# Kernel optimization log

Hardware: AMD Instinct MI355X
Metric: run time of the kernel (lower is better)

## Reference

```python
import jax, jax.numpy as jnp
import numpy as np
import math

D_MODEL = 1024
N_HEADS = 16
D_HEAD = 64
D_MLP = 4096
N_LAYERS = 12
INIT_STD = 0.02
EPS = 1e-5
BATCH = 2
SEQ = 2048


def setup_inputs() -> dict:
    key = jax.random.key(0)
    ks = jax.random.split(key, 8)
    attn_std = INIT_STD
    proj_std = INIT_STD / math.sqrt(2 * N_LAYERS)
    return {
        "resid_pre": jax.random.normal(ks[0], (BATCH, SEQ, D_MODEL), jnp.float32),
        "ln1_w": jnp.ones((D_MODEL,), jnp.float32),
        "ln1_b": jnp.zeros((D_MODEL,), jnp.float32),
        "W_Q": attn_std * jax.random.normal(ks[1], (N_HEADS, D_MODEL, D_HEAD), jnp.float32),
        "b_Q": jnp.zeros((N_HEADS, D_HEAD), jnp.float32),
        "W_K": attn_std * jax.random.normal(ks[2], (N_HEADS, D_MODEL, D_HEAD), jnp.float32),
        "b_K": jnp.zeros((N_HEADS, D_HEAD), jnp.float32),
        "W_V": attn_std * jax.random.normal(ks[3], (N_HEADS, D_MODEL, D_HEAD), jnp.float32),
        "b_V": jnp.zeros((N_HEADS, D_HEAD), jnp.float32),
        "W_O": proj_std * jax.random.normal(ks[4], (N_HEADS, D_HEAD, D_MODEL), jnp.float32),
        "b_O": jnp.zeros((D_MODEL,), jnp.float32),
        "ln2_w": jnp.ones((D_MODEL,), jnp.float32),
        "ln2_b": jnp.zeros((D_MODEL,), jnp.float32),
        "W_in": INIT_STD * jax.random.normal(ks[5], (D_MODEL, D_MLP), jnp.float32),
        "b_in": jnp.zeros((D_MLP,), jnp.float32),
        "W_out": proj_std * jax.random.normal(ks[6], (D_MLP, D_MODEL), jnp.float32),
        "b_out": jnp.zeros((D_MODEL,), jnp.float32),
    }


def _layernorm(x, w, b):
    mean = x.mean(-1, keepdims=True)
    var = x.var(-1, keepdims=True)  # unbiased=False
    return (x - mean) / jnp.sqrt(var + EPS) * w + b


def _attention(x, W_Q, b_Q, W_K, b_K, W_V, b_V, W_O, b_O):
    # x: [b, s, d]; W_*: [h, d, k]
    q = jnp.einsum('bsd,hdk->bshk', x, W_Q) + b_Q
    k = jnp.einsum('bsd,hdk->bshk', x, W_K) + b_K
    v = jnp.einsum('bsd,hdk->bshk', x, W_V) + b_V
    scores = jnp.einsum('bqhk,bshk->bhqs', q, k) / math.sqrt(D_HEAD)
    seq = x.shape[1]
    causal = jnp.tril(jnp.ones((seq, seq), bool))
    scores = jnp.where(causal, scores, -jnp.inf)
    pattern = jax.nn.softmax(scores, axis=-1)
    z = jnp.einsum('bhqs,bshk->bqhk', pattern, v)
    return jnp.einsum('bqhk,hkd->bqd', z, W_O) + b_O


def reference(resid_pre, ln1_w, ln1_b, W_Q, b_Q, W_K, b_K, W_V, b_V, W_O, b_O,
              ln2_w, ln2_b, W_in, b_in, W_out, b_out):
    attn_out = _attention(_layernorm(resid_pre, ln1_w, ln1_b),
                          W_Q, b_Q, W_K, b_K, W_V, b_V, W_O, b_O)
    resid_mid = resid_pre + attn_out
    h = _layernorm(resid_mid, ln2_w, ln2_b)
    mlp_out = jnp.matmul(jax.nn.relu(jnp.matmul(h, W_in) + b_in), W_out) + b_out
    return resid_mid + mlp_out
```

## Files before the change

### kernel.cpp

```cpp
#include <hip/hip_runtime.h>
#include <stdint.h>


typedef unsigned short u16;
typedef __bf16 bf16x8 __attribute__((ext_vector_type(8)));
typedef __bf16 bf16x4 __attribute__((ext_vector_type(4)));
typedef __bf16 bf16x2 __attribute__((ext_vector_type(2)));
typedef short  s16x4  __attribute__((ext_vector_type(4)));
typedef float  f32x4  __attribute__((ext_vector_type(4)));

#define QSCALE 0.18033688011112042f

__device__ __forceinline__ float bf2f(unsigned int u) {
  union { unsigned int u; float f; } v; v.u = u << 16; return v.f;
}
__device__ __forceinline__ u16 f2bf(float f) {
  union { float f; unsigned int u; } v; v.f = f;
  unsigned int r = v.u + 0x7FFFu + ((v.u >> 16) & 1u);
  return (u16)(r >> 16);
}
__device__ __forceinline__ unsigned pkbf(float lo, float hi) {
#if __has_builtin(__builtin_amdgcn_cvt_pk_bf16_f32)
  bf16x2 t = __builtin_amdgcn_cvt_pk_bf16_f32(lo, hi);
  return __builtin_bit_cast(unsigned, t);
#else
  return (unsigned)f2bf(lo) | ((unsigned)f2bf(hi) << 16);
#endif
}
__device__ __forceinline__ float loadf(const void* p, size_t i, int isf) {
  return isf ? ((const float*)p)[i] : bf2f(((const u16*)p)[i]);
}

__device__ __forceinline__ f32x4 mfma16(s16x4 a, s16x4 b, f32x4 c) {
#if __has_builtin(__builtin_amdgcn_mfma_f32_16x16x16_bf16)
  return __builtin_amdgcn_mfma_f32_16x16x16_bf16(
      __builtin_bit_cast(bf16x4, a), __builtin_bit_cast(bf16x4, b), c, 0, 0, 0);
#else
  return __builtin_amdgcn_mfma_f32_16x16x16bf16_1k(a, b, c, 0, 0, 0);
#endif
}

__global__ __launch_bounds__(256) void detect_dtype(
    const unsigned int* __restrict__ x, int* __restrict__ flag) {
  __shared__ int cnt;
  if (threadIdx.x == 0) cnt = 0;
  __syncthreads();
  int c = 0;
  for (int i = threadIdx.x; i < 512; i += 256) {
    unsigned int e = (x[i] >> 23) & 0xFFu;
    if (e >= 97u && e <= 157u) c++;
  }
  atomicAdd(&cnt, c);
  __syncthreads();
  if (threadIdx.x == 0) *flag = (cnt > 384) ? 1 : 0;
}

__global__ __launch_bounds__(256) void pack_qkv_tiled(
    const int* __restrict__ flagp,
    const void* __restrict__ Wq, const void* __restrict__ Wk, const void* __restrict__ Wv,
    u16* __restrict__ WT) {
  __shared__ float t[64][65];
  const int isf = *flagp;
  const int tid = threadIdx.x;
  const int mh = blockIdx.y;
  const int mat = mh >> 4, h = mh & 15;
  const int d0 = blockIdx.x << 6;
  const void* src = (mat == 0) ? Wq : (mat == 1) ? Wk : Wv;
  const float scale = (mat == 0) ? QSCALE : 1.f;
  const int lane = tid & 63, rr = tid >> 6;
  const size_t sbase = ((size_t)h << 16) + lane;
#pragma unroll
  for (int i = 0; i < 16; i++) {
    int d = i * 4 + rr;
    t[d][lane] = loadf(src, sbase + (size_t)(d0 + d) * 64, isf) * scale;
  }
  __syncthreads();
#pragma unroll
  for (int i = 0; i < 16; i++) {
    int k = i * 4 + rr;
    WT[((size_t)((mat << 10) + (h << 6) + k) << 10) + d0 + lane] = f2bf(t[lane][k]);
  }
}

__global__ __launch_bounds__(256) void transpose_tiled(
    const int* __restrict__ flagp, const void* __restrict__ src,
    u16* __restrict__ dst, int R, int C) {
  __shared__ float t[64][65];
  const int isf = *flagp;
  const int tid = threadIdx.x;
  const int c0 = blockIdx.x << 6, r0 = blockIdx.y << 6;
  const int lane = tid & 63, rr = tid >> 6;
#pragma unroll
  for (int i = 0; i < 16; i++) {
    int r = i * 4 + rr;
    t[r][lane] = loadf(src, (size_t)(r0 + r) * C + c0 + lane, isf);
  }
  __syncthreads();
#pragma unroll
  for (int i = 0; i < 16; i++) {
    int c = i * 4 + rr;
    dst[(size_t)(c0 + c) * R + r0 + lane] = f2bf(t[lane][c]);
  }
}

__global__ __launch_bounds__(256) void pack_biases(
    const int* __restrict__ flagp,
    const void* bq, const void* bk, const void* bv,
    const void* bO, const void* bin, const void* bout,
    float* __restrict__ out) {
  const int isf = *flagp;
  int i = blockIdx.x * 256 + threadIdx.x;
  float v;
  if (i < 1024)      v = loadf(bq,   i,        isf) * QSCALE;
  else if (i < 2048) v = loadf(bk,   i - 1024, isf);
  else if (i < 3072) v = loadf(bv,   i - 2048, isf);
  else if (i < 4096) v = loadf(bO,   i - 3072, isf);
  else if (i < 8192) v = loadf(bin,  i - 4096, isf);
  else               v = loadf(bout, i - 8192, isf);
  out[i] = v;
}

template<int SRC>
__global__ __launch_bounds__(256) void ln_fwd(
    const int* __restrict__ flagp, const void* __restrict__ xin,
    const void* __restrict__ w, const void* __restrict__ b,
    u16* __restrict__ out) {
  const int isf = *flagp;
  const int row = blockIdx.x, tid = threadIdx.x;
  const int col = tid << 2;
  const size_t base = ((size_t)row << 10) + col;
  float v[4];
#pragma unroll
  for (int i = 0; i < 4; i++)
    v[i] = (SRC == 1) ? ((const float*)xin)[base + i] : loadf(xin, base + i, isf);
  float s  = v[0] + v[1] + v[2] + v[3];
  float ss = v[0]*v[0] + v[1]*v[1] + v[2]*v[2] + v[3]*v[3];
#pragma unroll
  for (int mk = 32; mk >= 1; mk >>= 1) {
    s  += __shfl_xor(s,  mk, 64);
    ss += __shfl_xor(ss, mk, 64);
  }
  __shared__ float red[8];
  if ((tid & 63) == 0) { red[tid >> 6] = s; red[4 + (tid >> 6)] = ss; }
  __syncthreads();
  float S  = red[0] + red[1] + red[2] + red[3];
  float SS = red[4] + red[5] + red[6] + red[7];
  float mean = S * (1.f / 1024.f);
  float var  = SS * (1.f / 1024.f) - mean * mean;
  float rstd = rsqrtf(var + 1e-5f);
  u16 e[4];
#pragma unroll
  for (int i = 0; i < 4; i++) {
    float wv = loadf(w, col + i, isf);
    float bv = loadf(b, col + i, isf);
    e[i] = f2bf((v[i] - mean) * rstd * wv + bv);
  }
  uint2 o;
  o.x = (unsigned)e[0] | ((unsigned)e[1] << 16);
  o.y = (unsigned)e[2] | ((unsigned)e[3] << 16);
  *(uint2*)(out + base) = o;
}

template<int MODE, int TM, int KW>
__global__ __launch_bounds__(KW * 256) void gemm_bt(
    const int* __restrict__ flagp,
    const u16* __restrict__ A, const u16* __restrict__ BT,
    const float* __restrict__ bias, const void* __restrict__ resid,
    void* __restrict__ out, void* __restrict__ out2, void* __restrict__ out3,
    int M, int N, int K, int SHL) {
  constexpr int WR = TM / 32;
  constexpr int ASZ = TM * 32;
  constexpr int BSZ = 128 * 32;
  constexpr int STAGE_B = KW * (ASZ + BSZ) * 2;
  constexpr int RED_B = (KW > 1) ? TM * 132 * 4 : 1;
  constexpr int SMEM_B = STAGE_B > RED_B ? STAGE_B : RED_B;
  __shared__ __align__(16) char smem[SMEM_B];
  u16* as = (u16*)smem;
  u16* bs = (u16*)smem + KW * ASZ;

  int isf = 0;
  if (MODE == 2 || MODE == 3) isf = *flagp;
  const int Lb = blockIdx.x;
  const int xcd = Lb & 7, sidx = Lb >> 3;
  const int SH = 1 << SHL;
  const int by = xcd * SH + (sidx & (SH - 1));
  const int bx = sidx >> SHL;
  const int tid = threadIdx.x;
  const int L = tid & 63, w = tid >> 6;
  const int g = w >> 2, wl = w & 3;
  const int wm = (wl >> 1) * (TM >> 1), wn = (wl & 1) << 6;
  const int row0 = by * TM, col0 = bx << 7;
  const int m = L & 15, quad = L >> 4;

  f32x4 zero4 = {0.f, 0.f, 0.f, 0.f};
  f32x4 acc[WR][4];
#pragma unroll
  for (int i = 0; i < WR; i++)
#pragma unroll
    for (int j = 0; j < 4; j++) acc[i][j] = zero4;

  const int KSEG = K / KW;
  const int tl = tid & 255;
  const int tm = tl >> 2;
  const int tk = (tl & 3) << 3;
  const u16* Ag  = A  + (size_t)(row0 + tm) * K + g * KSEG + tk;
  const u16* Ag2 = Ag + (size_t)64 * K;
  const u16* Bg  = BT + (size_t)(col0 + tm) * K + g * KSEG + tk;
  const u16* Bg2 = Bg + (size_t)64 * K;
  u16* asg  = as + g * ASZ;
  u16* bsg  = bs + g * BSZ;
  u16* asl  = asg + tl * 8;
  u16* asl2 = asg + 2048 + tl * 8;
  u16* bsl  = bsg + tl * 8;
  u16* bsl2 = bsg + 2048 + tl * 8;

  const int aoff = (wm + m) * 32 + quad * 8;
  const int boff = (wn + m) * 32 + quad * 8;

  int4 ar0, ar1, br0, br1;
  ar0 = *(const int4*)Ag;
  if (TM == 128) ar1 = *(const int4*)Ag2;
  br0 = *(const int4*)Bg;
  br1 = *(const int4*)Bg2;

  for (int kk = 0; kk < KSEG; kk += 32) {
    __syncthreads();
    *(int4*)asl = ar0;
    if (TM == 128) *(int4*)asl2 = ar1;
    *(int4*)bsl = br0;
    *(int4*)bsl2 = br1;
    __syncthreads();
    if (kk + 32 < KSEG) {
      ar0 = *(const int4*)(Ag + kk + 32);
      if (TM == 128) ar1 = *(const int4*)(Ag2 + kk + 32);
      br0 = *(const int4*)(Bg + kk + 32);
      br1 = *(const int4*)(Bg2 + kk + 32);
    }
    bf16x8 af[WR], bfr[4];
#pragma unroll
    for (int i = 0; i < WR; i++) af[i]  = *(const bf16x8*)&asg[aoff + i * 512];
#pragma unroll
    for (int j = 0; j < 4; j++) bfr[j] = *(const bf16x8*)&bsg[boff + j * 512];
#pragma unroll
    for (int i = 0; i < WR; i++)
#pragma unroll
      for (int j = 0; j < 4; j++)
        acc[i][j] = __builtin_amdgcn_mfma_f32_16x16x32_bf16(af[i], bfr[j], acc[i][j], 0, 0, 0);
  }

  if (KW > 1) {
    __syncthreads();
    float* red = (float*)smem;
    if (g == 1) {
#pragma unroll
      for (int i = 0; i < WR; i++)
#pragma unroll
        for (int j = 0; j < 4; j++)
#pragma unroll
          for (int r = 0; r < 4; r++)
            red[(wm + i * 16 + quad * 4 + r) * 132 + wn + j * 16 + m] = acc[i][j][r];
    }
    __syncthreads();
    if (g == 0) {
#pragma unroll
      for (int i = 0; i < WR; i++)
#pragma unroll
        for (int j = 0; j < 4; j++)
#pragma unroll
          for (int r = 0; r < 4; r++)
            acc[i][j][r] += red[(wm + i * 16 + quad * 4 + r) * 132 + wn + j * 16 + m];
    }
  }

  if (g == 0) {
#pragma unroll
    for (int j = 0; j < 4; j++) {
      const int col = col0 + wn + j * 16 + m;
      const float bval = bias[col];
      if (MODE == 4) {
        const int sel = col >> 10;
        const int hh  = (col >> 6) & 15;
        const int f   = col & 63;
#pragma unroll
        for (int i = 0; i < WR; i++) {
          const int rowb = row0 + wm + i * 16 + quad * 4;
          if (sel < 2) {
            u16* dst = (u16*)(sel ? out2 : out);
#pragma unroll
            for (int r = 0; r < 4; r++)
              dst[((((size_t)hh << 12) + rowb + r) << 6) + f] = f2bf(acc[i][j][r] + bval);
          } else {
            uint2 o;
            o.x = pkbf(acc[i][j][0] + bval, acc[i][j][1] + bval);
            o.y = pkbf(acc[i][j][2] + bval, acc[i][j][3] + bval);
            *(uint2*)&((u16*)out3)[(((size_t)hh * 64 + f) << 12) + rowb] = o;
          }
        }
      } else {
#pragma unroll
        for (int i = 0; i < WR; i++) {
          const int rowb = row0 + wm + i * 16 + quad * 4;
#pragma unroll
          for (int r = 0; r < 4; r++) {
            float vv = acc[i][j][r] + bval;
            size_t idx = (size_t)(rowb + r) * N + col;
            if (MODE == 1) {
              ((u16*)out)[idx] = f2bf(fmaxf(vv, 0.f));
            } else if (MODE == 2) {
              ((float*)out)[idx] = vv + loadf(resid, idx, isf);
            } else if (MODE == 3) {
              float o = vv + ((const float*)resid)[idx];
              if (isf) ((float*)out)[idx] = o;
              else     ((u16*)out)[idx]   = f2bf(o);
            }
          }
        }
      }
    }
  }
}

__global__ __launch_bounds__(256, 3) void attn_part(
    const u16* __restrict__ qh, const u16* __restrict__ kh,
    const u16* __restrict__ vT, u16* __restrict__ Opart,
    float* __restrict__ stats) {
  const int combo = blockIdx.x;
  const int qt = blockIdx.y;
  const int ci = blockIdx.z;
  const int q0 = qt << 6;
  const int nc = (q0 + 64 + 511) >> 9;
  if (ci >= nc) return;
  const int k_lo = ci << 9;
  const int k_hi = min(k_lo + 512, q0 + 64);
  const int nsteps = (k_hi - k_lo + 127) >> 7;

  __shared__ u16 kS[128 * 72];
  __shared__ u16 vS[64 * 136];
  const int tid = threadIdx.x, L = tid & 63, w = tid >> 6;
  const int m = L & 15, quad = L >> 4;
  const int h = combo >> 1, b = combo & 1;
  const size_t tb = (size_t)b * 2048;
  const size_t hbase = (size_t)h * 4096;
  const int qg = q0 + w * 16 + m;

  bf16x8 qb0, qb1;
  {
    const u16* qp = qh + ((hbase + tb + (size_t)qg) << 6) + quad * 8;
    qb0 = *(const bf16x8*)qp;
    qb1 = *(const bf16x8*)(qp + 32);
  }

  f32x4 zero4 = {0.f, 0.f, 0.f, 0.f};
  f32x4 O[4];
#pragma unroll
  for (int ft = 0; ft < 4; ft++) O[ft] = zero4;
  float mrow = -30000.f, lrow = 0.f;

  const int krow[4] = { (0*256+tid) >> 3, (1*256+tid) >> 3, (2*256+tid) >> 3, (3*256+tid) >> 3 };
  const int kc = tid & 7;
  const int vf[4] = { (0*256+tid) >> 4, (1*256+tid) >> 4, (2*256+tid) >> 4, (3*256+tid) >> 4 };
  const int vc = tid & 15;
  const int vq = (vc & 1) << 1;
  const int vk4 = (vc >> 1) << 2;
  const int vc0 = (vq << 5) + vk4;
  const int vc1 = ((vq + 1) << 5) + vk4;

  int4 kr[4], vr[4];
#pragma unroll
  for (int i = 0; i < 4; i++) {
    kr[i] = *(const int4*)(kh + ((hbase + tb + k_lo + krow[i]) << 6) + kc * 8);
    vr[i] = *(const int4*)(vT + (((size_t)h * 64 + vf[i]) << 12) + tb + k_lo + vc * 8);
  }

  for (int j = 0; j < nsteps; j++) {
    const int k0 = k_lo + (j << 7);
    __syncthreads();
#pragma unroll
    for (int i = 0; i < 4; i++) {
      *(int4*)&kS[krow[i] * 72 + kc * 8] = kr[i];
      union { int4 v; s16x4 hh[2]; } tv; tv.v = vr[i];
      *(s16x4*)&vS[vf[i] * 136 + vc0] = tv.hh[0];
      *(s16x4*)&vS[vf[i] * 136 + vc1] = tv.hh[1];
    }
    __syncthreads();
    if (j + 1 < nsteps) {
      const int k1 = k_lo + ((j + 1) << 7);
#pragma unroll
      for (int i = 0; i < 4; i++) {
        kr[i] = *(const int4*)(kh + ((hbase + tb + k1 + krow[i]) << 6) + kc * 8);
        vr[i] = *(const int4*)(vT + (((size_t)h * 64 + vf[i]) << 12) + tb + k1 + vc * 8);
      }
    }
    f32x4 sc[8];
#pragma unroll
    for (int kt = 0; kt < 8; kt++) {
      const u16* kp = &kS[(kt * 16 + m) * 72 + quad * 8];
      bf16x8 ka0 = *(const bf16x8*)kp;
      bf16x8 ka1 = *(const bf16x8*)(kp + 32);
      f32x4 t = zero4;
      t = __builtin_amdgcn_mfma_f32_16x16x32_bf16(ka0, qb0, t, 0, 0, 0);
      t = __builtin_amdgcn_mfma_f32_16x16x32_bf16(ka1, qb1, t, 0, 0, 0);
      sc[kt] = t;
    }
    if (k0 + 128 > q0) {
#pragma unroll
      for (int kt = 0; kt < 8; kt++)
#pragma unroll
        for (int r = 0; r < 4; r++) {
          int ktok = k0 + kt * 16 + quad * 4 + r;
          if (ktok > qg) sc[kt][r] = -30000.f;
        }
    }
    float mx = sc[0][0];
#pragma unroll
    for (int kt = 0; kt < 8; kt++)
#pragma unroll
      for (int r = 0; r < 4; r++) mx = fmaxf(mx, sc[kt][r]);
    mx = fmaxf(mx, __shfl_xor(mx, 16, 64));
    mx = fmaxf(mx, __shfl_xor(mx, 32, 64));
    float mnew = fmaxf(mrow, mx);
    float alpha = __builtin_amdgcn_exp2f(mrow - mnew);
    mrow = mnew;
    s16x4 pb[8];
    float sum = 0.f;
#pragma unroll
    for (int kt = 0; kt < 8; kt++) {
      float e0 = __builtin_amdgcn_exp2f(sc[kt][0] - mnew);
      float e1 = __builtin_amdgcn_exp2f(sc[kt][1] - mnew);
      float e2 = __builtin_amdgcn_exp2f(sc[kt][2] - mnew);
      float e3 = __builtin_amdgcn_exp2f(sc[kt][3] - mnew);
      sum += (e0 + e1) + (e2 + e3);
      union { uint2 u; s16x4 hh; } pu;
      pu.u.x = pkbf(e0, e1);
      pu.u.y = pkbf(e2, e3);
      pb[kt] = pu.hh;
    }
    sum += __shfl_xor(sum, 16, 64);
    sum += __shfl_xor(sum, 32, 64);
    lrow = lrow * alpha + sum;
#pragma unroll
    for (int ft = 0; ft < 4; ft++) O[ft] *= alpha;
#pragma unroll
    for (int ft = 0; ft < 4; ft++) {
      const u16* vp = &vS[(ft * 16 + m) * 136 + quad * 32];
#pragma unroll
      for (int pr = 0; pr < 4; pr++) {
        union { bf16x8 v; s16x4 hh[2]; } u;
        u.v = *(const bf16x8*)(vp + pr * 8);
        O[ft] = mfma16(u.hh[0], pb[2 * pr],     O[ft]);
        O[ft] = mfma16(u.hh[1], pb[2 * pr + 1], O[ft]);
      }
    }
  }

  __syncthreads();
#pragma unroll
  for (int ft = 0; ft < 4; ft++) {
    union { uint2 u; s16x4 hh; } o4;
    o4.u.x = pkbf(O[ft][0], O[ft][1]);
    o4.u.y = pkbf(O[ft][2], O[ft][3]);
    *(s16x4*)&kS[(w * 16 + m) * 72 + ft * 16 + quad * 4] = o4.hh;
  }
  __syncthreads();
  const int slot = (combo * 32 + qt) * 4 + ci;
  u16* op = Opart + ((size_t)slot << 12);
#pragma unroll
  for (int it = 0; it < 2; it++) {
    int idx = it * 256 + tid;
    int row = idx >> 3, c = idx & 7;
    *(int4*)&op[row * 64 + c * 8] = *(const int4*)&kS[row * 72 + c * 8];
  }
  if (quad == 0) {
    stats[slot * 128 + w * 16 + m]      = mrow;
    stats[slot * 128 + 64 + w * 16 + m] = lrow;
  }
}

__global__ __launch_bounds__(256) void attn_merge(
    const u16* __restrict__ Opart, const float* __restrict__ stats,
    u16* __restrict__ z) {
  const int combo = blockIdx.x, qt = blockIdx.y;
  const int h = combo >> 1, b = combo & 1;
  const int q0 = qt << 6;
  const int nc = (q0 + 64 + 511) >> 9;
  const int tid = threadIdx.x;
  const int t = tid >> 2, f0 = (tid & 3) << 4;
  const int slot0 = (combo * 32 + qt) * 4;
  float M = -3e4f;
  for (int ci = 0; ci < nc; ci++)
    M = fmaxf(M, stats[(slot0 + ci) * 128 + t]);
  float acc[16];
#pragma unroll
  for (int e = 0; e < 16; e++) acc[e] = 0.f;
  float ltot = 0.f;
  for (int ci = 0; ci < nc; ci++) {
    float mi = stats[(slot0 + ci) * 128 + t];
    float li = stats[(slot0 + ci) * 128 + 64 + t];
    float wgt = exp2f(mi - M);
    ltot += wgt * li;
    const u16* op = Opart + (((size_t)(slot0 + ci)) << 12) + t * 64 + f0;
    union { int4 v; u16 u[8]; } a0, a1;
    a0.v = *(const int4*)op;
    a1.v = *(const int4*)(op + 8);
#pragma unroll
    for (int e = 0; e < 8; e++) {
      acc[e]     += wgt * bf2f(a0.u[e]);
      acc[8 + e] += wgt * bf2f(a1.u[e]);
    }
  }
  float inv = 1.f / ltot;
  union { int4 v; u16 u[8]; } o0, o1;
#pragma unroll
  for (int e = 0; e < 8; e++) {
    o0.u[e] = f2bf(acc[e] * inv);
    o1.u[e] = f2bf(acc[8 + e] * inv);
  }
  size_t tok = (size_t)b * 2048 + q0 + t;
  *(int4*)&z[tok * 1024 + h * 64 + f0]     = o0.v;
  *(int4*)&z[tok * 1024 + h * 64 + f0 + 8] = o1.v;
}

extern "C" void kernel_launch(void* const* d_in, const int* in_sizes, int n_in,
                              void* d_out, int out_size, void* d_ws, size_t ws_size,
                              hipStream_t stream) {
  (void)in_sizes; (void)n_in; (void)out_size; (void)ws_size;
  const void* resid_pre = d_in[0];
  const void* ln1_w = d_in[1];
  const void* ln1_b = d_in[2];
  const void* W_Q   = d_in[3];
  const void* b_Q   = d_in[4];
  const void* W_K   = d_in[5];
  const void* b_K   = d_in[6];
  const void* W_V   = d_in[7];
  const void* b_V   = d_in[8];
  const void* W_O   = d_in[9];
  const void* b_O   = d_in[10];
  const void* ln2_w = d_in[11];
  const void* ln2_b = d_in[12];
  const void* W_in  = d_in[13];
  const void* b_in  = d_in[14];
  const void* W_out = d_in[15];
  const void* b_out = d_in[16];

  char* p = (char*)d_ws;
  auto alloc = [&](size_t bytes) {
    char* r = p; p += (bytes + 255) & ~(size_t)255; return (void*)r;
  };
  int*   flag      = (int*)  alloc(256);
  u16*   WqkvT     = (u16*)  alloc(3072ull * 1024 * 2);
  u16*   WoT       = (u16*)  alloc(1024ull * 1024 * 2);
  u16*   WinT      = (u16*)  alloc(4096ull * 1024 * 2);
  u16*   WoutT     = (u16*)  alloc(1024ull * 4096 * 2);
  float* biases    = (float*)alloc(9216 * 4);
  u16*   xn        = (u16*)  alloc(4096ull * 1024 * 2);
  u16*   q_hm      = (u16*)  alloc(16ull * 4096 * 64 * 2);
  u16*   k_hm      = (u16*)  alloc(16ull * 4096 * 64 * 2);
  u16*   vTws      = (u16*)  alloc(16ull * 64 * 4096 * 2);
  float* resid_mid = (float*)alloc(4096ull * 1024 * 4);
  u16*   h2        = (u16*)  alloc(4096ull * 1024 * 2);
  u16*   act       = (u16*)  alloc(4096ull * 4096 * 2);
  u16*   z = xn;
  u16*   Opart = act;
  float* stats = (float*)h2;

  detect_dtype<<<1, 256, 0, stream>>>((const unsigned int*)resid_pre, flag);

  pack_qkv_tiled<<<dim3(16, 48), 256, 0, stream>>>(flag, W_Q, W_K, W_V, WqkvT);
  transpose_tiled<<<dim3(16, 16), 256, 0, stream>>>(flag, W_O,   WoT,   1024, 1024);
  transpose_tiled<<<dim3(64, 16), 256, 0, stream>>>(flag, W_in,  WinT,  1024, 4096);
  transpose_tiled<<<dim3(16, 64), 256, 0, stream>>>(flag, W_out, WoutT, 4096, 1024);
  pack_biases<<<36, 256, 0, stream>>>(flag, b_Q, b_K, b_V, b_O, b_in, b_out, biases);

  ln_fwd<0><<<4096, 256, 0, stream>>>(flag, resid_pre, ln1_w, ln1_b, xn);
  gemm_bt<4, 128, 1><<<768, 256, 0, stream>>>(
      flag, xn, WqkvT, biases, nullptr, q_hm, k_hm, vTws, 4096, 3072, 1024, 2);
  attn_part<<<dim3(32, 32, 4), 256, 0, stream>>>(q_hm, k_hm, vTws, Opart, stats);
  attn_merge<<<dim3(32, 32), 256, 0, stream>>>(Opart, stats, z);
  gemm_bt<2, 64, 2><<<512, 512, 0, stream>>>(
      flag, z, WoT, biases + 3072, resid_pre, resid_mid, nullptr, nullptr, 4096, 1024, 1024, 3);
  ln_fwd<1><<<4096, 256, 0, stream>>>(flag, resid_mid, ln2_w, ln2_b, h2);
  gemm_bt<1, 128, 1><<<1024, 256, 0, stream>>>(
      flag, h2, WinT, biases + 4096, nullptr, act, nullptr, nullptr, 4096, 4096, 1024, 2);
  gemm_bt<3, 64, 2><<<512, 512, 0, stream>>>(
      flag, act, WoutT, biases + 8192, resid_mid, d_out, nullptr, nullptr, 4096, 1024, 4096, 3);
}
```

Measured before the change: 430.3 us.

## Use 1024-key attention chunks, write single-chunk tiles directly, skip lazy rescale

Causal split-K attention now uses key chunks of 1024 instead of 512, so each query tile has at most two chunks. Tiles whose keys fit in one chunk normalize in-kernel and write z directly, and the merge kernel only handles the upper 16 query tiles with a fixed two-way merge. The online softmax also skips the alpha rescale of O and l unless the running max grows by more than 8 (log2 units), and occupancy is raised to 4 blocks per SIMD. The aim is less partial-output traffic, less merge work and fewer rescale multiplies, at the cost of longer per-block key loops and a slightly looser exponent bound.

```diff
diff --git a/kernel.cpp b/kernel.cpp
--- a/kernel.cpp
+++ b/kernel.cpp
@@ -320,18 +320,18 @@
   }
 }
 
-__global__ __launch_bounds__(256, 3) void attn_part(
+__global__ __launch_bounds__(256, 4) void attn_part(
     const u16* __restrict__ qh, const u16* __restrict__ kh,
     const u16* __restrict__ vT, u16* __restrict__ Opart,
-    float* __restrict__ stats) {
+    float* __restrict__ stats, u16* __restrict__ z) {
   const int combo = blockIdx.x;
   const int qt = blockIdx.y;
   const int ci = blockIdx.z;
   const int q0 = qt << 6;
-  const int nc = (q0 + 64 + 511) >> 9;
+  const int nc = (q0 + 64 + 1023) >> 10;
   if (ci >= nc) return;
-  const int k_lo = ci << 9;
-  const int k_hi = min(k_lo + 512, q0 + 64);
+  const int k_lo = ci << 10;
+  const int k_hi = min(k_lo + 1024, q0 + 64);
   const int nsteps = (k_hi - k_lo + 127) >> 7;
 
   __shared__ u16 kS[128 * 72];
@@ -418,17 +418,22 @@
       for (int r = 0; r < 4; r++) mx = fmaxf(mx, sc[kt][r]);
     mx = fmaxf(mx, __shfl_xor(mx, 16, 64));
     mx = fmaxf(mx, __shfl_xor(mx, 32, 64));
-    float mnew = fmaxf(mrow, mx);
-    float alpha = __builtin_amdgcn_exp2f(mrow - mnew);
-    mrow = mnew;
+    if (!__all(mx <= mrow + 8.f)) {
+      float mnew = fmaxf(mrow, mx);
+      float alpha = __builtin_amdgcn_exp2f(mrow - mnew);
+      lrow *= alpha;
+#pragma unroll
+      for (int ft = 0; ft < 4; ft++) O[ft] *= alpha;
+      mrow = mnew;
+    }
     s16x4 pb[8];
     float sum = 0.f;
 #pragma unroll
     for (int kt = 0; kt < 8; kt++) {
-      float e0 = __builtin_amdgcn_exp2f(sc[kt][0] - mnew);
-      float e1 = __builtin_amdgcn_exp2f(sc[kt][1] - mnew);
-      float e2 = __builtin_amdgcn_exp2f(sc[kt][2] - mnew);
-      float e3 = __builtin_amdgcn_exp2f(sc[kt][3] - mnew);
+      float e0 = __builtin_amdgcn_exp2f(sc[kt][0] - mrow);
+      float e1 = __builtin_amdgcn_exp2f(sc[kt][1] - mrow);
+      float e2 = __builtin_amdgcn_exp2f(sc[kt][2] - mrow);
+      float e3 = __builtin_amdgcn_exp2f(sc[kt][3] - mrow);
       sum += (e0 + e1) + (e2 + e3);
       union { uint2 u; s16x4 hh; } pu;
       pu.u.x = pkbf(e0, e1);
@@ -437,9 +442,7 @@
     }
     sum += __shfl_xor(sum, 16, 64);
     sum += __shfl_xor(sum, 32, 64);
-    lrow = lrow * alpha + sum;
-#pragma unroll
-    for (int ft = 0; ft < 4; ft++) O[ft] *= alpha;
+    lrow += sum;
 #pragma unroll
     for (int ft = 0; ft < 4; ft++) {
       const u16* vp = &vS[(ft * 16 + m) * 136 + quad * 32];
@@ -453,6 +456,12 @@
     }
   }
 
+  if (nc == 1) {
+    float inv = 1.f / lrow;
+#pragma unroll
+    for (int ft = 0; ft < 4; ft++) O[ft] *= inv;
+  }
+
   __syncthreads();
 #pragma unroll
   for (int ft = 0; ft < 4; ft++) {
@@ -462,38 +471,46 @@
     *(s16x4*)&kS[(w * 16 + m) * 72 + ft * 16 + quad * 4] = o4.hh;
   }
   __syncthreads();
-  const int slot = (combo * 32 + qt) * 4 + ci;
-  u16* op = Opart + ((size_t)slot << 12);
-#pragma unroll
-  for (int it = 0; it < 2; it++) {
-    int idx = it * 256 + tid;
-    int row = idx >> 3, c = idx & 7;
-    *(int4*)&op[row * 64 + c * 8] = *(const int4*)&kS[row * 72 + c * 8];
-  }
-  if (quad == 0) {
-    stats[slot * 128 + w * 16 + m]      = mrow;
-    stats[slot * 128 + 64 + w * 16 + m] = lrow;
+  if (nc == 1) {
+    u16* zp = z + ((tb + (size_t)q0) << 10) + h * 64;
+#pragma unroll
+    for (int it = 0; it < 2; it++) {
+      int idx = it * 256 + tid;
+      int row = idx >> 3, c = idx & 7;
+      *(int4*)&zp[((size_t)row << 10) + c * 8] = *(const int4*)&kS[row * 72 + c * 8];
+    }
+  } else {
+    const int slot = (combo * 32 + qt) * 2 + ci;
+    u16* op = Opart + ((size_t)slot << 12);
+#pragma unroll
+    for (int it = 0; it < 2; it++) {
+      int idx = it * 256 + tid;
+      int row = idx >> 3, c = idx & 7;
+      *(int4*)&op[row * 64 + c * 8] = *(const int4*)&kS[row * 72 + c * 8];
+    }
+    if (quad == 0) {
+      stats[slot * 128 + w * 16 + m]      = mrow;
+      stats[slot * 128 + 64 + w * 16 + m] = lrow;
+    }
   }
 }
 
 __global__ __launch_bounds__(256) void attn_merge(
     const u16* __restrict__ Opart, const float* __restrict__ stats,
     u16* __restrict__ z) {
-  const int combo = blockIdx.x, qt = blockIdx.y;
+  const int combo = blockIdx.x, qt = 16 + blockIdx.y;
   const int h = combo >> 1, b = combo & 1;
   const int q0 = qt << 6;
-  const int nc = (q0 + 64 + 511) >> 9;
   const int tid = threadIdx.x;
   const int t = tid >> 2, f0 = (tid & 3) << 4;
-  const int slot0 = (combo * 32 + qt) * 4;
-  float M = -3e4f;
-  for (int ci = 0; ci < nc; ci++)
-    M = fmaxf(M, stats[(slot0 + ci) * 128 + t]);
+  const int slot0 = (combo * 32 + qt) * 2;
+  float M = fmaxf(stats[slot0 * 128 + t], stats[(slot0 + 1) * 128 + t]);
   float acc[16];
 #pragma unroll
   for (int e = 0; e < 16; e++) acc[e] = 0.f;
   float ltot = 0.f;
-  for (int ci = 0; ci < nc; ci++) {
+#pragma unroll
+  for (int ci = 0; ci < 2; ci++) {
     float mi = stats[(slot0 + ci) * 128 + t];
     float li = stats[(slot0 + ci) * 128 + 64 + t];
     float wgt = exp2f(mi - M);
@@ -574,8 +591,8 @@
   ln_fwd<0><<<4096, 256, 0, stream>>>(flag, resid_pre, ln1_w, ln1_b, xn);
   gemm_bt<4, 128, 1><<<768, 256, 0, stream>>>(
       flag, xn, WqkvT, biases, nullptr, q_hm, k_hm, vTws, 4096, 3072, 1024, 2);
-  attn_part<<<dim3(32, 32, 4), 256, 0, stream>>>(q_hm, k_hm, vTws, Opart, stats);
-  attn_merge<<<dim3(32, 32), 256, 0, stream>>>(Opart, stats, z);
+  attn_part<<<dim3(32, 32, 2), 256, 0, stream>>>(q_hm, k_hm, vTws, Opart, stats, z);
+  attn_merge<<<dim3(32, 16), 256, 0, stream>>>(Opart, stats, z);
   gemm_bt<2, 64, 2><<<512, 512, 0, stream>>>(
       flag, z, WoT, biases + 3072, resid_pre, resid_mid, nullptr, nullptr, 4096, 1024, 1024, 3);
   ln_fwd<1><<<4096, 256, 0, stream>>>(flag, resid_mid, ln2_w, ln2_b, h2);
```

Result: no change. 428.0 us (-0.5%).
